# Kernel tuning notes

Hardware: AMD Instinct MI355X
Metric: run time of the kernel (lower is better)

## Reference

```python
import math
import jax, jax.numpy as jnp
import numpy as np

MODEL_DIM = 2048
NUM_HEADS = 16
HEAD_DIM = MODEL_DIM // NUM_HEADS
B, T = 4, 2048


def setup_inputs() -> dict:
    key = jax.random.key(0)
    ks = jax.random.split(key, 9)
    s = 0.02
    d = MODEL_DIM
    return {
        "x": jax.random.normal(ks[0], (B, T, d), dtype=jnp.float32),
        "wq": jax.random.normal(ks[1], (d, d), dtype=jnp.float32) * s,
        "bq": jnp.zeros((d,), dtype=jnp.float32),
        "wk": jax.random.normal(ks[2], (d, d), dtype=jnp.float32) * s,
        "bk": jnp.zeros((d,), dtype=jnp.float32),
        "wv": jax.random.normal(ks[3], (d, d), dtype=jnp.float32) * s,
        "bv": jnp.zeros((d,), dtype=jnp.float32),
        "wo": jax.random.normal(ks[4], (d, d), dtype=jnp.float32) * s,
        "bo": jnp.zeros((d,), dtype=jnp.float32),
    }


def reference(x, wq, bq, wk, bk, wv, bv, wo, bo):
    b, t, d = x.shape
    h, hd = NUM_HEADS, HEAD_DIM
    scale = 1.0 / math.sqrt(hd)
    # torch Linear: y = x @ W^T + b
    q = (x @ wq.T + bq).reshape(b, t, h, hd).transpose(0, 2, 1, 3)  # [B,H,T,hd]
    k = (x @ wk.T + bk).reshape(b, t, h, hd).transpose(0, 2, 1, 3)
    v = (x @ wv.T + bv).reshape(b, t, h, hd).transpose(0, 2, 1, 3)
    scores = jnp.einsum("bhqd,bhkd->bhqk", q, k) * scale  # [B,H,T,T]
    mask = jnp.tril(jnp.ones((t, t), dtype=bool))
    scores = jnp.where(mask[None, None], scores, -jnp.inf)
    probs = jax.nn.softmax(scores, axis=-1)
    out = jnp.einsum("bhqk,bhkd->bhqd", probs, v)  # [B,H,T,hd]
    out = out.transpose(0, 2, 1, 3).reshape(b, t, d)
    out = out @ wo.T + bo
    return (out, k, v)
```

## Files before the change

### kernel.cpp

```cpp
#include <hip/hip_runtime.h>
#include <hip/hip_bf16.h>
#include <stdint.h>

typedef __attribute__((ext_vector_type(8))) short short8;
typedef __attribute__((ext_vector_type(4))) float f32x4;

#define DEVI __device__ __forceinline__

DEVI unsigned short f2bf(float f) {
  union { float f; unsigned int u; } c; c.f = f;
  unsigned int u = c.u;
  u += 0x7fffu + ((u >> 16) & 1u);
  return (unsigned short)(u >> 16);
}

DEVI void gl_lds16(const void* gsrc, void* lds) {
  __builtin_amdgcn_global_load_lds(
      (const __attribute__((address_space(1))) unsigned int*)gsrc,
      (__attribute__((address_space(3))) unsigned int*)lds, 16, 0, 0);
}

#define MFMA(a, b, c) __builtin_amdgcn_mfma_f32_16x16x32_bf16((a), (b), (c), 0, 0, 0)
#define BAR()  __builtin_amdgcn_s_barrier()
#define SCHED0() __builtin_amdgcn_sched_barrier(0)

__global__ void cvt_all(const float* __restrict__ x, unsigned short* __restrict__ xb,
                        const float* __restrict__ w0, const float* __restrict__ w1,
                        const float* __restrict__ w2, const float* __restrict__ w3,
                        unsigned short* __restrict__ o0, unsigned short* __restrict__ o1,
                        unsigned short* __restrict__ o2, unsigned short* __restrict__ o3) {
  const int sel = blockIdx.y;
  const float* in;
  unsigned short* out;
  if (sel < 4) { in = x + (size_t)sel * 4194304; out = xb + (size_t)sel * 4194304; }
  else if (sel == 4) { in = w0; out = o0; }
  else if (sel == 5) { in = w1; out = o1; }
  else if (sel == 6) { in = w2; out = o2; }
  else               { in = w3; out = o3; }
  const int stride = gridDim.x * blockDim.x;
  for (int i = blockIdx.x * blockDim.x + threadIdx.x; i < 1048576; i += stride) {
    const float4 v = ((const float4*)in)[i];
    ushort4 o;
    o.x = f2bf(v.x); o.y = f2bf(v.y); o.z = f2bf(v.z); o.w = f2bf(v.w);
    ((ushort4*)out)[i] = o;
  }
}


template<int MODE>
__global__ __launch_bounds__(512, 2)
void gemm8p(const unsigned short* __restrict__ A,
            const unsigned short* __restrict__ Bw,
            const float* __restrict__ bq,
            const float* __restrict__ bk,
            const float* __restrict__ bv,
            float* __restrict__ Kf,
            float* __restrict__ Vf,
            unsigned short* __restrict__ Qpk,
            unsigned short* __restrict__ Kpk,
            unsigned short* __restrict__ Vpk,
            float* __restrict__ Cf,
            int M, int N, int K)
{
  __shared__ unsigned short S[2][32768];
  const int tid  = threadIdx.x;
  const int lane = tid & 63;
  const int wid  = tid >> 6;
  const int l15  = lane & 15, l4 = lane >> 4;
  const int wm   = wid >> 2, wn = wid & 3;

  const int q   = blockIdx.x;
  const int xcd = q & 7;
  const int idx = q >> 3;
  const int bm = (xcd * 4 + (idx & 3)) * 256;
  const int bn = (idx >> 2) * 256;

  const unsigned short* Asrc = A  + (size_t)(bm + (wid >> 1) * 16 + l15) * K + (wid & 1) * 32 + l4 * 8;
  const unsigned short* Bsrc = Bw + (size_t)(bn + (wid >> 1) * 16 + l15) * K + (wid & 1) * 32 + l4 * 8;

  const int nKt   = K >> 6;
  const int HTmax = nKt * 4;

  auto stage_ht = [&](int g) {
    if (g >= HTmax) return;
    const int t = g >> 2, sub = g & 3, buf = t & 1, k0 = t << 6;
#pragma unroll
    for (int cc = 0; cc < 2; ++cc) {
      if (sub >= 2) {
        const int c = (sub - 2) * 2 + cc;
        gl_lds16(Asrc + (size_t)(c * 64) * K + k0,
                 &S[buf][c * 4096 + wid * 512 + lane * 8]);
      } else {
        const int c = sub * 2 + cc;
        gl_lds16(Bsrc + (size_t)(c * 64) * K + k0,
                 &S[buf][16384 + c * 4096 + wid * 512 + lane * 8]);
      }
    }
  };

#pragma unroll
  for (int g = 0; g < 7; ++g) stage_ht(g);
  asm volatile("s_waitcnt vmcnt(6)" ::: "memory");
  SCHED0();
  BAR();

  f32x4 acc[8][4] = {};
  short8 a[4][2], b[4][2];

  for (int t = 0; t < nKt; ++t) {
    const unsigned short* Sb = S[t & 1];
    const int P = t * 4;

#pragma unroll
    for (int i = 0; i < 4; ++i)
#pragma unroll
      for (int ks = 0; ks < 2; ++ks)
        a[i][ks] = *(const short8*)&Sb[((wm * 8 + i) * 2 + ks) * 512 + lane * 8];
#pragma unroll
    for (int j = 0; j < 4; ++j)
#pragma unroll
      for (int ks = 0; ks < 2; ++ks)
        b[j][ks] = *(const short8*)&Sb[16384 + ((wn * 4 + j) * 2 + ks) * 512 + lane * 8];
    stage_ht(P + 7);
    BAR();
    asm volatile("s_waitcnt lgkmcnt(0)" ::: "memory");
    SCHED0();
    __builtin_amdgcn_s_setprio(1);
#pragma unroll
    for (int i = 0; i < 4; ++i)
#pragma unroll
      for (int j = 0; j < 2; ++j)
#pragma unroll
        for (int ks = 0; ks < 2; ++ks)
          acc[i][j] = MFMA(a[i][ks], b[j][ks], acc[i][j]);
    __builtin_amdgcn_s_setprio(0);
    BAR();

    stage_ht(P + 8);
    BAR();
    __builtin_amdgcn_s_setprio(1);
#pragma unroll
    for (int i = 0; i < 4; ++i)
#pragma unroll
      for (int j = 0; j < 2; ++j)
#pragma unroll
        for (int ks = 0; ks < 2; ++ks)
          acc[i][2 + j] = MFMA(a[i][ks], b[2 + j][ks], acc[i][2 + j]);
    __builtin_amdgcn_s_setprio(0);
    BAR();

#pragma unroll
    for (int i = 0; i < 4; ++i)
#pragma unroll
      for (int ks = 0; ks < 2; ++ks)
        a[i][ks] = *(const short8*)&Sb[((wm * 8 + 4 + i) * 2 + ks) * 512 + lane * 8];
    stage_ht(P + 9);
    BAR();
    asm volatile("s_waitcnt lgkmcnt(0)" ::: "memory");
    SCHED0();
    __builtin_amdgcn_s_setprio(1);
#pragma unroll
    for (int i = 0; i < 4; ++i)
#pragma unroll
      for (int j = 0; j < 2; ++j)
#pragma unroll
        for (int ks = 0; ks < 2; ++ks)
          acc[4 + i][j] = MFMA(a[i][ks], b[j][ks], acc[4 + i][j]);
    __builtin_amdgcn_s_setprio(0);
    BAR();

    stage_ht(P + 10);
    if (t < nKt - 2)       { asm volatile("s_waitcnt vmcnt(6)" ::: "memory"); SCHED0(); }
    else if (t == nKt - 2) { asm volatile("s_waitcnt vmcnt(0)" ::: "memory"); SCHED0(); }
    BAR();
    __builtin_amdgcn_s_setprio(1);
#pragma unroll
    for (int i = 0; i < 4; ++i)
#pragma unroll
      for (int j = 0; j < 2; ++j)
#pragma unroll
        for (int ks = 0; ks < 2; ++ks)
          acc[4 + i][2 + j] = MFMA(a[i][ks], b[2 + j][ks], acc[4 + i][2 + j]);
    __builtin_amdgcn_s_setprio(0);
    BAR();
  }

  const int rbase = l4 * 4;
#pragma unroll
  for (int m = 0; m < 8; ++m) {
    const int row0 = bm + wm * 128 + m * 16 + rbase;
#pragma unroll
    for (int n = 0; n < 4; ++n) {
      const int col6 = bn + wn * 64 + n * 16 + l15;
      if constexpr (MODE == 3) {
        const float bb = bq[col6];
#pragma unroll
        for (int r = 0; r < 4; ++r)
          Cf[(size_t)(row0 + r) * N + col6] = acc[m][n][r] + bb;
      } else {
        const int sel = col6 >> 11;
        const int col = col6 & 2047;
        const float bb = (sel == 0 ? bq : sel == 1 ? bk : bv)[col];
        float vv[4];
#pragma unroll
        for (int r = 0; r < 4; ++r) vv[r] = acc[m][n][r] + bb;
        const int bI = row0 >> 11, t0 = row0 & 2047;
        const int h = col >> 7, e = col & 127;
        const size_t hb = ((size_t)(bI * 16 + h)) * 262144;
        if (sel == 0) {
          const size_t qb = hb + (size_t)(t0 >> 4) * 2048 + (e >> 5) * 512
                          + (t0 & 15) * 32 + (e & 31);
#pragma unroll
          for (int r = 0; r < 4; ++r) Qpk[qb + (size_t)r * 32] = f2bf(vv[r]);
        } else if (sel == 1) {
          const size_t idx2 = hb + (size_t)t0 * 128 + e;
          const size_t qb = hb + (size_t)(t0 >> 4) * 2048 + (e >> 5) * 512
                          + (t0 & 15) * 32 + (e & 31);
#pragma unroll
          for (int r = 0; r < 4; ++r) {
            Kf[idx2 + (size_t)r * 128] = vv[r];
            Kpk[qb + (size_t)r * 32] = f2bf(vv[r]);
          }
        } else {
          const size_t idx2 = hb + (size_t)t0 * 128 + e;
#pragma unroll
          for (int r = 0; r < 4; ++r) Vf[idx2 + (size_t)r * 128] = vv[r];
          const size_t vb = hb + (size_t)(t0 >> 6) * 8192 + (size_t)(e >> 4) * 1024
                          + ((t0 >> 5) & 1) * 512 + (e & 15) * 32 + (t0 & 31);
          ushort4 pk;
          pk.x = f2bf(vv[0]); pk.y = f2bf(vv[1]);
          pk.z = f2bf(vv[2]); pk.w = f2bf(vv[3]);
          *(ushort4*)&Vpk[vb] = pk;
        }
      }
    }
  }
}

__global__ __launch_bounds__(256, 2)
void attn_fwd(const unsigned short* __restrict__ Qf,
              const unsigned short* __restrict__ Kf,
              const unsigned short* __restrict__ Vf,
              unsigned short* __restrict__ Ab)
{
  constexpr float scale = 0.08838834764831843f;
  __shared__ unsigned short Pl[4][32][72];

  const int bid = blockIdx.x;
  const int xcd = bid & 7;
  const int idx = bid >> 3;
  const int bh  = xcd * 8 + (idx & 7);
  const int prI = idx >> 3;
  const int tid = threadIdx.x;
  const int wid = tid >> 6, lane = tid & 63;
  const int p   = prI * 4 + wid;
  const int bI = bh >> 4, h = bh & 15;
  const int lr = lane & 15, lg = lane >> 4;
  const int lfo = lr * 32 + lg * 8;

  const unsigned short* Qh = Qf + (size_t)bh * 262144;
  const unsigned short* Kp = Kf + (size_t)bh * 262144;
  const unsigned short* Vp = Vf + (size_t)bh * 262144;

  for (int pass = 0; pass < 2; ++pass) {
    const int strip = pass ? p : (63 - p);
    const int qw = strip * 32;
    const unsigned short* Qp = Qh + (size_t)(qw >> 4) * 2048;

    short8 qf[2][4];
#pragma unroll
    for (int m = 0; m < 2; ++m)
#pragma unroll
      for (int ks = 0; ks < 4; ++ks)
        qf[m][ks] = *(const short8*)&Qp[m * 2048 + ks * 512 + lfo];

    f32x4 o[2][8] = {};
    float mrun[2][4], lrun[2][4];
#pragma unroll
    for (int m = 0; m < 2; ++m)
#pragma unroll
      for (int r = 0; r < 4; ++r) { mrun[m][r] = -1e30f; lrun[m][r] = 0.f; }

    const int nfull = qw >> 6;
    for (int kt = 0; kt <= nfull; ++kt) {
      const int kv0 = kt * 64;
      const bool diag = (kt == nfull);
      const unsigned short* Kt = Kp + (size_t)(kv0 >> 4) * 2048;
      const unsigned short* Vt = Vp + (size_t)(kv0 >> 6) * 8192;

      short8 kf[4][4];
#pragma unroll
      for (int n = 0; n < 4; ++n)
#pragma unroll
        for (int ks = 0; ks < 4; ++ks)
          kf[n][ks] = *(const short8*)&Kt[n * 2048 + ks * 512 + lfo];
      f32x4 s[2][4] = {};
      __builtin_amdgcn_s_setprio(1);
#pragma unroll
      for (int ks = 0; ks < 4; ++ks)
#pragma unroll
        for (int m = 0; m < 2; ++m)
#pragma unroll
          for (int n = 0; n < 4; ++n)
            s[m][n] = MFMA(qf[m][ks], kf[n][ks], s[m][n]);
      __builtin_amdgcn_s_setprio(0);

      short8 vf[2][8];
#pragma unroll
      for (int ks2 = 0; ks2 < 2; ++ks2)
#pragma unroll
        for (int dt = 0; dt < 8; ++dt)
          vf[ks2][dt] = *(const short8*)&Vt[dt * 1024 + ks2 * 512 + lfo];

      float tmax[2][4];
#pragma unroll
      for (int m = 0; m < 2; ++m)
#pragma unroll
        for (int r = 0; r < 4; ++r) tmax[m][r] = -1e30f;
#pragma unroll
      for (int m = 0; m < 2; ++m)
#pragma unroll
        for (int n = 0; n < 4; ++n) {
          const int kg = kv0 + n * 16 + lr;
#pragma unroll
          for (int r = 0; r < 4; ++r) {
            float sv = s[m][n][r] * scale;
            if (diag) {
              const int qg = qw + m * 16 + lg * 4 + r;
              sv = (kg <= qg) ? sv : -1e30f;
            }
            s[m][n][r] = sv;
            tmax[m][r] = fmaxf(tmax[m][r], sv);
          }
        }
#pragma unroll
      for (int m = 0; m < 2; ++m)
#pragma unroll
        for (int r = 0; r < 4; ++r)
#pragma unroll
          for (int off = 8; off >= 1; off >>= 1)
            tmax[m][r] = fmaxf(tmax[m][r], __shfl_xor(tmax[m][r], off));

      float grow = -1e30f;
#pragma unroll
      for (int m = 0; m < 2; ++m)
#pragma unroll
        for (int r = 0; r < 4; ++r)
          grow = fmaxf(grow, tmax[m][r] - mrun[m][r]);
      if (!__all(grow <= 8.0f)) {
#pragma unroll
        for (int m = 0; m < 2; ++m)
#pragma unroll
          for (int r = 0; r < 4; ++r) {
            const float mnew  = fmaxf(mrun[m][r], tmax[m][r]);
            const float alpha = __expf(mrun[m][r] - mnew);
            mrun[m][r] = mnew;
            lrun[m][r] *= alpha;
#pragma unroll
            for (int d = 0; d < 8; ++d) o[m][d][r] *= alpha;
          }
      }
#pragma unroll
      for (int m = 0; m < 2; ++m) {
        float ls[4] = {0.f, 0.f, 0.f, 0.f};
#pragma unroll
        for (int n = 0; n < 4; ++n)
#pragma unroll
          for (int r = 0; r < 4; ++r) {
            const float pv = __expf(s[m][n][r] - mrun[m][r]);
            s[m][n][r] = pv;
            ls[r] += pv;
          }
#pragma unroll
        for (int r = 0; r < 4; ++r) {
#pragma unroll
          for (int off = 8; off >= 1; off >>= 1) ls[r] += __shfl_xor(ls[r], off);
          lrun[m][r] += ls[r];
        }
#pragma unroll
        for (int n = 0; n < 4; ++n)
#pragma unroll
          for (int r = 0; r < 4; ++r)
            Pl[wid][m * 16 + lg * 4 + r][n * 16 + lr] = f2bf(s[m][n][r]);
      }
#pragma unroll
      for (int ks2 = 0; ks2 < 2; ++ks2) {
        short8 pa[2];
#pragma unroll
        for (int m = 0; m < 2; ++m)
          pa[m] = *(const short8*)&Pl[wid][m * 16 + lr][ks2 * 32 + lg * 8];
        __builtin_amdgcn_s_setprio(1);
#pragma unroll
        for (int dt = 0; dt < 8; ++dt)
#pragma unroll
          for (int m = 0; m < 2; ++m)
            o[m][dt] = MFMA(pa[m], vf[ks2][dt], o[m][dt]);
        __builtin_amdgcn_s_setprio(0);
      }
    }
#pragma unroll
    for (int m = 0; m < 2; ++m)
#pragma unroll
      for (int r = 0; r < 4; ++r) {
        const float inv = 1.0f / lrun[m][r];
        const int t = qw + m * 16 + lg * 4 + r;
        unsigned short* dst = Ab + ((size_t)(bI * 2048 + t)) * 2048 + h * 128;
#pragma unroll
        for (int dt = 0; dt < 8; ++dt)
          dst[dt * 16 + lr] = f2bf(o[m][dt][r] * inv);
      }
  }
}

extern "C" void kernel_launch(void* const* d_in, const int* in_sizes, int n_in,
                              void* d_out, int out_size, void* d_ws, size_t ws_size,
                              hipStream_t stream) {
  const float* x  = (const float*)d_in[0];
  const float* wq = (const float*)d_in[1];
  const float* bq = (const float*)d_in[2];
  const float* wk = (const float*)d_in[3];
  const float* bk = (const float*)d_in[4];
  const float* wv = (const float*)d_in[5];
  const float* bv = (const float*)d_in[6];
  const float* wo = (const float*)d_in[7];
  const float* bo = (const float*)d_in[8];

  float* out  = (float*)d_out;
  float* kout = out + (size_t)16777216;
  float* vout = out + (size_t)33554432;

  unsigned short* xb  = (unsigned short*)d_ws;
  unsigned short* wqb = xb  + 16777216;
  unsigned short* wkb = wqb + 4194304;
  unsigned short* wvb = wkb + 4194304;
  unsigned short* wob = wvb + 4194304;
  unsigned short* Qw  = wob + 4194304;
  unsigned short* Kw  = Qw  + 16777216;
  unsigned short* Vfw = Kw  + 16777216;
  unsigned short* Aw  = Vfw + 16777216;

  const int M = 8192, K = 2048;

  cvt_all<<<dim3(256, 8), 256, 0, stream>>>(x, xb, wq, wk, wv, wo,
                                            wqb, wkb, wvb, wob);

  gemm8p<0><<<dim3(768), 512, 0, stream>>>(xb, wqb, bq, bk, bv,
                                           kout, vout, Qw, Kw, Vfw,
                                           nullptr, M, 6144, K);

  attn_fwd<<<dim3(512), 256, 0, stream>>>(Qw, Kw, Vfw, Aw);

  gemm8p<3><<<dim3(256), 512, 0, stream>>>(Aw, wob, bo, nullptr, nullptr,
                                           nullptr, nullptr, nullptr, nullptr, nullptr,
                                           out, M, 2048, K);
}
```

Baseline: 484.3 us.

## Make QKV GEMM persistent over three tiles, prefetching next tile's B during current

The QKV projection GEMM now launches 256 blocks that each process three output tiles sharing the same A row-block. The next tile's weight tiles are prefetched into LDS during the tail of the current tile's K loop. The aim is to hide the pipeline ramp-up and drain between tiles and to reuse the A rows from cache, replacing the 768-block launch. In exchange, the epilogue stores of one tile no longer overlap with other blocks' compute, and the tile-to-XCD mapping changes.

Result: slower. 574.5 us (+18.6%).

```diff
diff --git a/kernel.cpp b/kernel.cpp
--- a/kernel.cpp
+++ b/kernel.cpp
@@ -47,7 +47,7 @@
 }
 
 
-template<int MODE>
+template<int MODE, int REPS>
 __global__ __launch_bounds__(512, 2)
 void gemm8p(const unsigned short* __restrict__ A,
             const unsigned short* __restrict__ Bw,
@@ -69,21 +69,29 @@
   const int l15  = lane & 15, l4 = lane >> 4;
   const int wm   = wid >> 2, wn = wid & 3;
 
-  const int q   = blockIdx.x;
-  const int xcd = q & 7;
-  const int idx = q >> 3;
-  const int bm = (xcd * 4 + (idx & 3)) * 256;
-  const int bn = (idx >> 2) * 256;
-
-  const unsigned short* Asrc = A  + (size_t)(bm + (wid >> 1) * 16 + l15) * K + (wid & 1) * 32 + l4 * 8;
-  const unsigned short* Bsrc = Bw + (size_t)(bn + (wid >> 1) * 16 + l15) * K + (wid & 1) * 32 + l4 * 8;
+  const int nblk  = gridDim.x;
+  const int chunk = (nblk * REPS) >> 3;
+  const int q     = blockIdx.x;
+  const int wg0 = (q & 7) * chunk + (q >> 3);
+  const int bm  = (wg0 & 31) * 256;
+  const unsigned short* Asrc = A + (size_t)(bm + (wid >> 1) * 16 + l15) * K + (wid & 1) * 32 + l4 * 8;
 
   const int nKt   = K >> 6;
   const int HTmax = nKt * 4;
 
-  auto stage_ht = [&](int g) {
-    if (g >= HTmax) return;
-    const int t = g >> 2, sub = g & 3, buf = t & 1, k0 = t << 6;
+  auto bsrc_of = [&](int rep) -> const unsigned short* {
+    const int g  = rep * nblk + q;
+    const int wg = (g & 7) * chunk + (g >> 3);
+    const int bn = (wg >> 5) * 256;
+    return Bw + (size_t)(bn + (wid >> 1) * 16 + l15) * K + (wid & 1) * 32 + l4 * 8;
+  };
+
+  auto stage_ht = [&](int g, const unsigned short* Bc, const unsigned short* Bn) {
+    int t = g >> 2;
+    const unsigned short* Bu = Bc;
+    int tt = t;
+    if (t >= nKt) { if (Bn == nullptr) return; tt = t - nKt; Bu = Bn; }
+    const int sub = g & 3, buf = t & 1, k0 = tt << 6;
 #pragma unroll
     for (int cc = 0; cc < 2; ++cc) {
       if (sub >= 2) {
@@ -92,145 +100,167 @@
                  &S[buf][c * 4096 + wid * 512 + lane * 8]);
       } else {
         const int c = sub * 2 + cc;
-        gl_lds16(Bsrc + (size_t)(c * 64) * K + k0,
+        gl_lds16(Bu + (size_t)(c * 64) * K + k0,
                  &S[buf][16384 + c * 4096 + wid * 512 + lane * 8]);
       }
     }
   };
 
-#pragma unroll
-  for (int g = 0; g < 7; ++g) stage_ht(g);
-  asm volatile("s_waitcnt vmcnt(6)" ::: "memory");
-  SCHED0();
-  BAR();
-
-  f32x4 acc[8][4] = {};
+  {
+    const unsigned short* B0 = bsrc_of(0);
+#pragma unroll
+    for (int g = 0; g < 7; ++g) stage_ht(g, B0, nullptr);
+  }
+
+  f32x4 acc[8][4];
   short8 a[4][2], b[4][2];
-
-  for (int t = 0; t < nKt; ++t) {
-    const unsigned short* Sb = S[t & 1];
-    const int P = t * 4;
-
-#pragma unroll
-    for (int i = 0; i < 4; ++i)
-#pragma unroll
-      for (int ks = 0; ks < 2; ++ks)
-        a[i][ks] = *(const short8*)&Sb[((wm * 8 + i) * 2 + ks) * 512 + lane * 8];
-#pragma unroll
-    for (int j = 0; j < 4; ++j)
-#pragma unroll
-      for (int ks = 0; ks < 2; ++ks)
-        b[j][ks] = *(const short8*)&Sb[16384 + ((wn * 4 + j) * 2 + ks) * 512 + lane * 8];
-    stage_ht(P + 7);
+  const f32x4 vzero = {0.f, 0.f, 0.f, 0.f};
+
+  for (int rep = 0; rep < REPS; ++rep) {
+    const unsigned short* Bc = bsrc_of(rep);
+    const unsigned short* Bn = (rep + 1 < REPS) ? bsrc_of(rep + 1) : nullptr;
+    const bool lastrep = (rep + 1 == REPS);
+
+    asm volatile("s_waitcnt vmcnt(6)" ::: "memory");
+    SCHED0();
     BAR();
-    asm volatile("s_waitcnt lgkmcnt(0)" ::: "memory");
-    SCHED0();
-    __builtin_amdgcn_s_setprio(1);
-#pragma unroll
-    for (int i = 0; i < 4; ++i)
-#pragma unroll
-      for (int j = 0; j < 2; ++j)
+#pragma unroll
+    for (int i = 0; i < 8; ++i)
+#pragma unroll
+      for (int j = 0; j < 4; ++j) acc[i][j] = vzero;
+
+    for (int t = 0; t < nKt; ++t) {
+      const unsigned short* Sb = S[t & 1];
+      const int P = t * 4;
+
+#pragma unroll
+      for (int i = 0; i < 4; ++i)
 #pragma unroll
         for (int ks = 0; ks < 2; ++ks)
-          acc[i][j] = MFMA(a[i][ks], b[j][ks], acc[i][j]);
-    __builtin_amdgcn_s_setprio(0);
-    BAR();
-
-    stage_ht(P + 8);
-    BAR();
-    __builtin_amdgcn_s_setprio(1);
-#pragma unroll
-    for (int i = 0; i < 4; ++i)
-#pragma unroll
-      for (int j = 0; j < 2; ++j)
+          a[i][ks] = *(const short8*)&Sb[((wm * 8 + i) * 2 + ks) * 512 + lane * 8];
+#pragma unroll
+      for (int j = 0; j < 4; ++j)
 #pragma unroll
         for (int ks = 0; ks < 2; ++ks)
-          acc[i][2 + j] = MFMA(a[i][ks], b[2 + j][ks], acc[i][2 + j]);
-    __builtin_amdgcn_s_setprio(0);
-    BAR();
-
-#pragma unroll
-    for (int i = 0; i < 4; ++i)
-#pragma unroll
-      for (int ks = 0; ks < 2; ++ks)
-        a[i][ks] = *(const short8*)&Sb[((wm * 8 + 4 + i) * 2 + ks) * 512 + lane * 8];
-    stage_ht(P + 9);
-    BAR();
-    asm volatile("s_waitcnt lgkmcnt(0)" ::: "memory");
-    SCHED0();
-    __builtin_amdgcn_s_setprio(1);
-#pragma unroll
-    for (int i = 0; i < 4; ++i)
-#pragma unroll
-      for (int j = 0; j < 2; ++j)
+          b[j][ks] = *(const short8*)&Sb[16384 + ((wn * 4 + j) * 2 + ks) * 512 + lane * 8];
+      stage_ht(P + 7, Bc, Bn);
+      BAR();
+      asm volatile("s_waitcnt lgkmcnt(0)" ::: "memory");
+      SCHED0();
+      __builtin_amdgcn_s_setprio(1);
+#pragma unroll
+      for (int i = 0; i < 4; ++i)
+#pragma unroll
+        for (int j = 0; j < 2; ++j)
+#pragma unroll
+          for (int ks = 0; ks < 2; ++ks)
+            acc[i][j] = MFMA(a[i][ks], b[j][ks], acc[i][j]);
+      __builtin_amdgcn_s_setprio(0);
+      BAR();
+
+      stage_ht(P + 8, Bc, Bn);
+      BAR();
+      __builtin_amdgcn_s_setprio(1);
+#pragma unroll
+      for (int i = 0; i < 4; ++i)
+#pragma unroll
+        for (int j = 0; j < 2; ++j)
+#pragma unroll
+          for (int ks = 0; ks < 2; ++ks)
+            acc[i][2 + j] = MFMA(a[i][ks], b[2 + j][ks], acc[i][2 + j]);
+      __builtin_amdgcn_s_setprio(0);
+      BAR();
+
+#pragma unroll
+      for (int i = 0; i < 4; ++i)
 #pragma unroll
         for (int ks = 0; ks < 2; ++ks)
-          acc[4 + i][j] = MFMA(a[i][ks], b[j][ks], acc[4 + i][j]);
-    __builtin_amdgcn_s_setprio(0);
-    BAR();
-
-    stage_ht(P + 10);
-    if (t < nKt - 2)       { asm volatile("s_waitcnt vmcnt(6)" ::: "memory"); SCHED0(); }
-    else if (t == nKt - 2) { asm volatile("s_waitcnt vmcnt(0)" ::: "memory"); SCHED0(); }
-    BAR();
-    __builtin_amdgcn_s_setprio(1);
-#pragma unroll
-    for (int i = 0; i < 4; ++i)
-#pragma unroll
-      for (int j = 0; j < 2; ++j)
-#pragma unroll
-        for (int ks = 0; ks < 2; ++ks)
-          acc[4 + i][2 + j] = MFMA(a[i][ks], b[2 + j][ks], acc[4 + i][2 + j]);
-    __builtin_amdgcn_s_setprio(0);
-    BAR();
-  }
-
-  const int rbase = l4 * 4;
-#pragma unroll
-  for (int m = 0; m < 8; ++m) {
-    const int row0 = bm + wm * 128 + m * 16 + rbase;
-#pragma unroll
-    for (int n = 0; n < 4; ++n) {
-      const int col6 = bn + wn * 64 + n * 16 + l15;
-      if constexpr (MODE == 3) {
-        const float bb = bq[col6];
-#pragma unroll
-        for (int r = 0; r < 4; ++r)
-          Cf[(size_t)(row0 + r) * N + col6] = acc[m][n][r] + bb;
+          a[i][ks] = *(const short8*)&Sb[((wm * 8 + 4 + i) * 2 + ks) * 512 + lane * 8];
+      stage_ht(P + 9, Bc, Bn);
+      BAR();
+      asm volatile("s_waitcnt lgkmcnt(0)" ::: "memory");
+      SCHED0();
+      __builtin_amdgcn_s_setprio(1);
+#pragma unroll
+      for (int i = 0; i < 4; ++i)
+#pragma unroll
+        for (int j = 0; j < 2; ++j)
+#pragma unroll
+          for (int ks = 0; ks < 2; ++ks)
+            acc[4 + i][j] = MFMA(a[i][ks], b[j][ks], acc[4 + i][j]);
+      __builtin_amdgcn_s_setprio(0);
+      BAR();
+
+      stage_ht(P + 10, Bc, Bn);
+      if (!lastrep) {
+        asm volatile("s_waitcnt vmcnt(6)" ::: "memory"); SCHED0();
       } else {
-        const int sel = col6 >> 11;
-        const int col = col6 & 2047;
-        const float bb = (sel == 0 ? bq : sel == 1 ? bk : bv)[col];
-        float vv[4];
-#pragma unroll
-        for (int r = 0; r < 4; ++r) vv[r] = acc[m][n][r] + bb;
-        const int bI = row0 >> 11, t0 = row0 & 2047;
-        const int h = col >> 7, e = col & 127;
-        const size_t hb = ((size_t)(bI * 16 + h)) * 262144;
-        if (sel == 0) {
-          const size_t qb = hb + (size_t)(t0 >> 4) * 2048 + (e >> 5) * 512
-                          + (t0 & 15) * 32 + (e & 31);
-#pragma unroll
-          for (int r = 0; r < 4; ++r) Qpk[qb + (size_t)r * 32] = f2bf(vv[r]);
-        } else if (sel == 1) {
-          const size_t idx2 = hb + (size_t)t0 * 128 + e;
-          const size_t qb = hb + (size_t)(t0 >> 4) * 2048 + (e >> 5) * 512
-                          + (t0 & 15) * 32 + (e & 31);
-#pragma unroll
-          for (int r = 0; r < 4; ++r) {
-            Kf[idx2 + (size_t)r * 128] = vv[r];
-            Kpk[qb + (size_t)r * 32] = f2bf(vv[r]);
+        if (t < nKt - 2)       { asm volatile("s_waitcnt vmcnt(6)" ::: "memory"); SCHED0(); }
+        else if (t == nKt - 2) { asm volatile("s_waitcnt vmcnt(0)" ::: "memory"); SCHED0(); }
+      }
+      BAR();
+      __builtin_amdgcn_s_setprio(1);
+#pragma unroll
+      for (int i = 0; i < 4; ++i)
+#pragma unroll
+        for (int j = 0; j < 2; ++j)
+#pragma unroll
+          for (int ks = 0; ks < 2; ++ks)
+            acc[4 + i][2 + j] = MFMA(a[i][ks], b[2 + j][ks], acc[4 + i][2 + j]);
+      __builtin_amdgcn_s_setprio(0);
+      BAR();
+    }
+
+    const int grt = rep * nblk + q;
+    const int wgr = (grt & 7) * chunk + (grt >> 3);
+    const int bn  = (wgr >> 5) * 256;
+    const int rbase = l4 * 4;
+#pragma unroll
+    for (int m = 0; m < 8; ++m) {
+      const int row0 = bm + wm * 128 + m * 16 + rbase;
+#pragma unroll
+      for (int n = 0; n < 4; ++n) {
+        const int col6 = bn + wn * 64 + n * 16 + l15;
+        if constexpr (MODE == 3) {
+          const float bb = bq[col6];
+#pragma unroll
+          for (int r = 0; r < 4; ++r)
+            Cf[(size_t)(row0 + r) * N + col6] = acc[m][n][r] + bb;
+        } else {
+          const int sel = col6 >> 11;
+          const int col = col6 & 2047;
+          const float bb = (sel == 0 ? bq : sel == 1 ? bk : bv)[col];
+          float vv[4];
+#pragma unroll
+          for (int r = 0; r < 4; ++r) vv[r] = acc[m][n][r] + bb;
+          const int bI = row0 >> 11, t0 = row0 & 2047;
+          const int h = col >> 7, e = col & 127;
+          const size_t hb = ((size_t)(bI * 16 + h)) * 262144;
+          if (sel == 0) {
+            const size_t qb = hb + (size_t)(t0 >> 4) * 2048 + (e >> 5) * 512
+                            + (t0 & 15) * 32 + (e & 31);
+#pragma unroll
+            for (int r = 0; r < 4; ++r) Qpk[qb + (size_t)r * 32] = f2bf(vv[r]);
+          } else if (sel == 1) {
+            const size_t idx2 = hb + (size_t)t0 * 128 + e;
+            const size_t qb = hb + (size_t)(t0 >> 4) * 2048 + (e >> 5) * 512
+                            + (t0 & 15) * 32 + (e & 31);
+#pragma unroll
+            for (int r = 0; r < 4; ++r) {
+              Kf[idx2 + (size_t)r * 128] = vv[r];
+              Kpk[qb + (size_t)r * 32] = f2bf(vv[r]);
+            }
+          } else {
+            const size_t idx2 = hb + (size_t)t0 * 128 + e;
+#pragma unroll
+            for (int r = 0; r < 4; ++r) Vf[idx2 + (size_t)r * 128] = vv[r];
+            const size_t vb = hb + (size_t)(t0 >> 6) * 8192 + (size_t)(e >> 4) * 1024
+                            + ((t0 >> 5) & 1) * 512 + (e & 15) * 32 + (t0 & 31);
+            ushort4 pk;
+            pk.x = f2bf(vv[0]); pk.y = f2bf(vv[1]);
+            pk.z = f2bf(vv[2]); pk.w = f2bf(vv[3]);
+            *(ushort4*)&Vpk[vb] = pk;
           }
-        } else {
-          const size_t idx2 = hb + (size_t)t0 * 128 + e;
-#pragma unroll
-          for (int r = 0; r < 4; ++r) Vf[idx2 + (size_t)r * 128] = vv[r];
-          const size_t vb = hb + (size_t)(t0 >> 6) * 8192 + (size_t)(e >> 4) * 1024
-                          + ((t0 >> 5) & 1) * 512 + (e & 15) * 32 + (t0 & 31);
-          ushort4 pk;
-          pk.x = f2bf(vv[0]); pk.y = f2bf(vv[1]);
-          pk.z = f2bf(vv[2]); pk.w = f2bf(vv[3]);
-          *(ushort4*)&Vpk[vb] = pk;
         }
       }
     }
@@ -444,13 +474,13 @@
   cvt_all<<<dim3(256, 8), 256, 0, stream>>>(x, xb, wq, wk, wv, wo,
                                             wqb, wkb, wvb, wob);
 
-  gemm8p<0><<<dim3(768), 512, 0, stream>>>(xb, wqb, bq, bk, bv,
-                                           kout, vout, Qw, Kw, Vfw,
-                                           nullptr, M, 6144, K);
+  gemm8p<0, 3><<<dim3(256), 512, 0, stream>>>(xb, wqb, bq, bk, bv,
+                                              kout, vout, Qw, Kw, Vfw,
+                                              nullptr, M, 6144, K);
 
   attn_fwd<<<dim3(512), 256, 0, stream>>>(Qw, Kw, Vfw, Aw);
 
-  gemm8p<3><<<dim3(256), 512, 0, stream>>>(Aw, wob, bo, nullptr, nullptr,
-                                           nullptr, nullptr, nullptr, nullptr, nullptr,
-                                           out, M, 2048, K);
-}
+  gemm8p<3, 1><<<dim3(256), 512, 0, stream>>>(Aw, wob, bo, nullptr, nullptr,
+                                              nullptr, nullptr, nullptr, nullptr, nullptr,
+                                              out, M, 2048, K);
+}
```
